# Optimization experiments

Measured on AMD Instinct MI355X. Metric: run time of the kernel, lower is better.

## Reference

```python
import jax, jax.numpy as jnp
import numpy as np

TEMPERATURE = 0.1
SIGMA = 1.0
NUM_CLASSES = 4
INF = 1e8
EPS = 1e-12


def _l2_normalize(x):
    n = jnp.sqrt(jnp.sum(x * x, axis=-1, keepdims=True))
    return x / jnp.maximum(n, EPS)


def _rbf_kernel(y, gamma):
    # y: [M, P] -> [M, M] exp(-gamma * ||yi - yj||^2)
    sq = jnp.sum(y * y, axis=-1)
    d2 = sq[:, None] + sq[None, :] - 2.0 * (y @ y.T)
    d2 = jnp.maximum(d2, 0.0)
    return jnp.exp(-gamma * d2)


def setup_inputs() -> dict:
    key = jax.random.key(0)
    k1, k2, k3, k4 = jax.random.split(key, 4)
    N, D = 2048, 512
    return {
        "z_i": jax.random.normal(k1, (N, D), dtype=jnp.float32),
        "z_j": jax.random.normal(k2, (N, D), dtype=jnp.float32),
        "labels": jax.random.randint(k3, (N,), 0, NUM_CLASSES, dtype=jnp.int64),
        "z_pos": jax.random.uniform(k4, (N, 1), dtype=jnp.float32),
    }


def reference(z_i, z_j, labels, z_pos):
    N = z_i.shape[0]
    zi = _l2_normalize(z_i)
    zj = _l2_normalize(z_j)

    eye_n = jnp.eye(N, dtype=zi.dtype)
    sim_zii = (zi @ zi.T) / TEMPERATURE - INF * eye_n
    sim_zjj = (zj @ zj.T) / TEMPERATURE - INF * eye_n
    sim_zij = (zi @ zj.T) / TEMPERATURE

    # label agreement mask over the 2N x 2N augmented batch
    labs = jax.nn.one_hot(labels, NUM_CLASSES, dtype=jnp.float32)
    L = jnp.concatenate([labs, labs], axis=0)          # [2N, C]
    eye_2n = jnp.eye(2 * N, dtype=jnp.float32)
    mask = (L @ L.T) * (1.0 - eye_2n)

    # RBF kernel weights over positional labels (detached in original)
    all_pos = jnp.tile(z_pos.reshape(N, -1), (2, 1))   # [2N, P]
    gamma = 1.0 / (2.0 * SIGMA ** 2)
    weights = _rbf_kernel(all_pos, gamma) * (1.0 - eye_2n)

    final_weights = weights * mask
    # NB: torch broadcasting divides column j by rowsum[j]; matrix is symmetric
    final_weights = final_weights / final_weights.sum(axis=1)

    top = jnp.concatenate([sim_zii, sim_zij], axis=1)
    bot = jnp.concatenate([sim_zij.T, sim_zjj], axis=1)
    sim_Z = jnp.concatenate([top, bot], axis=0)        # [2N, 2N]

    log_sim_Z = jax.nn.log_softmax(sim_Z, axis=1)
    loss = (-1.0 / N) * jnp.sum(log_sim_Z * final_weights)
    return loss
```

## Files before the change

### kernel.cpp

```cpp
#include <hip/hip_runtime.h>
#include <hip/hip_bf16.h>

#define D 512
#define INV_T 10.0f
#define INF_VAL 1e8f

#define BM 128
#define BN 128
#define BK 64
#define KSTEPS (D / BK)
#define NTB 32
#define NBLK (NTB * (NTB + 1) / 2)
#define NCHUNK 64

typedef short bf16x8 __attribute__((ext_vector_type(8)));
typedef float f32x4 __attribute__((ext_vector_type(4)));

typedef __attribute__((address_space(3))) unsigned int lds_uint;
typedef __attribute__((address_space(1))) unsigned int gbl_uint;

__device__ __forceinline__ void async_copy16(const ushort* gsrc, ushort* ldst) {
  __builtin_amdgcn_global_load_lds((const gbl_uint*)gsrc, (lds_uint*)ldst, 16, 0, 0);
}

__device__ inline float wave_reduce_sum(float v) {
#pragma unroll
  for (int off = 32; off > 0; off >>= 1) v += __shfl_xor(v, off);
  return v;
}

__device__ __forceinline__ ushort f2bf(float x) {
  __hip_bfloat16 h = __float2bfloat16(x);
  return *reinterpret_cast<ushort*>(&h);
}

__global__ __launch_bounds__(256) void k_prep(const float* __restrict__ zi,
                                              const float* __restrict__ zj,
                                              ushort* __restrict__ zb,
                                              const int* __restrict__ labels,
                                              const float* __restrict__ zpos,
                                              float* __restrict__ sinv, int N) {
  int b = blockIdx.x;
  if (b < 1024) {
    int wv = threadIdx.x >> 6, lane = threadIdx.x & 63;
    int row = b * 4 + wv;
    const float* src = (row < N) ? (zi + (size_t)row * D) : (zj + (size_t)(row - N) * D);
    const float4* s4 = reinterpret_cast<const float4*>(src);
    float4 v0 = s4[lane];
    float4 v1 = s4[lane + 64];
    float ss = 0.f;
    ss = fmaf(v0.x, v0.x, ss); ss = fmaf(v0.y, v0.y, ss);
    ss = fmaf(v0.z, v0.z, ss); ss = fmaf(v0.w, v0.w, ss);
    ss = fmaf(v1.x, v1.x, ss); ss = fmaf(v1.y, v1.y, ss);
    ss = fmaf(v1.z, v1.z, ss); ss = fmaf(v1.w, v1.w, ss);
    ss = wave_reduce_sum(ss);
    float sc = 1.0f / fmaxf(sqrtf(ss), 1e-12f);
    ushort4 o0 = {f2bf(v0.x * sc), f2bf(v0.y * sc), f2bf(v0.z * sc), f2bf(v0.w * sc)};
    ushort4 o1 = {f2bf(v1.x * sc), f2bf(v1.y * sc), f2bf(v1.z * sc), f2bf(v1.w * sc)};
    ushort4* dst = reinterpret_cast<ushort4*>(zb + (size_t)row * D);
    dst[lane] = o0;
    dst[lane + 64] = o1;
  } else {
    __shared__ float scratch[4];
    int j = b - 1024;
    int lj = labels[j];
    float pj = zpos[j];
    float s = 0.f;
    for (int i = threadIdx.x; i < N; i += 256) {
      if (labels[i] == lj) {
        float d = zpos[i] - pj;
        s += __expf(-0.5f * d * d);
      }
    }
    s = wave_reduce_sum(s);
    int lane = threadIdx.x & 63, wv = threadIdx.x >> 6;
    if (lane == 0) scratch[wv] = s;
    __syncthreads();
    if (threadIdx.x == 0) {
      float t = scratch[0] + scratch[1] + scratch[2] + scratch[3];
      sinv[j] = 1.0f / (2.0f * t - 1.0f);
    }
  }
}

__global__ __launch_bounds__(256) void k_tt(const int* __restrict__ labels,
                                            const float* __restrict__ zpos,
                                            const float* __restrict__ sinv,
                                            float* __restrict__ tt, int N) {
  __shared__ float scratch[4];
  int i = blockIdx.x;
  int li = labels[i];
  float pi = zpos[i];
  float s = 0.f;
  for (int j = threadIdx.x; j < N; j += 256) {
    if (labels[j] == li) {
      float d = zpos[j] - pi;
      s += __expf(-0.5f * d * d) * sinv[j];
    }
  }
  s = wave_reduce_sum(s);
  int lane = threadIdx.x & 63, wv = threadIdx.x >> 6;
  if (lane == 0) scratch[wv] = s;
  __syncthreads();
  if (threadIdx.x == 0) {
    tt[i] = scratch[0] + scratch[1] + scratch[2] + scratch[3];
  }
}

__global__ __launch_bounds__(256, 2) void k_gemm(
    const ushort* __restrict__ zb, const int* __restrict__ labels,
    const float* __restrict__ zpos, const float* __restrict__ sinv,
    float* __restrict__ s_ws, float* __restrict__ c_ws, int N) {
  __shared__ __align__(16) ushort sT[2][2][BM * BK];

  const int tid = threadIdx.x;
  const int lane = tid & 63;
  const int wv = tid >> 6;
  const int wr = wv >> 1;
  const int wc = wv & 1;
  const int colq = lane & 15;
  const int laneg = lane >> 4;
  const int twoN = 2 * N;

  const int bid = blockIdx.x;
  int L = (bid & 7) * (NBLK / 8) + (bid >> 3);
  int u = L, rt = 0;
  while (u >= NTB - rt) { u -= NTB - rt; ++rt; }
  const int ct = rt + u;
  const bool diag = (rt == ct);
  const int rowBase = rt * BM;
  const int colBase = ct * BN;

  const int srow = lane >> 3;
  const int sslot = (lane & 7) ^ srow;

  f32x4 acc[4][4] = {};

  {
#pragma unroll
    for (int q = 0; q < 4; ++q) {
      int rloc = wv * 32 + q * 8;
      async_copy16(zb + (size_t)(rowBase + rloc + srow) * D + 0 * BK + sslot * 8,
                   (ushort*)sT[0][0] + rloc * BK);
      if (!diag)
        async_copy16(zb + (size_t)(colBase + rloc + srow) * D + 0 * BK + sslot * 8,
                     (ushort*)sT[0][1] + rloc * BK);
    }
  }
  __syncthreads();

  int cur = 0;
#pragma unroll
  for (int kt = 0; kt < KSTEPS; ++kt) {
    if (kt + 1 < KSTEPS) {
#pragma unroll
      for (int q = 0; q < 4; ++q) {
        int rloc = wv * 32 + q * 8;
        async_copy16(zb + (size_t)(rowBase + rloc + srow) * D + (kt + 1) * BK + sslot * 8,
                     (ushort*)sT[cur ^ 1][0] + rloc * BK);
        if (!diag)
          async_copy16(zb + (size_t)(colBase + rloc + srow) * D + (kt + 1) * BK + sslot * 8,
                       (ushort*)sT[cur ^ 1][1] + rloc * BK);
      }
    }

    const char* Ab = reinterpret_cast<const char*>(sT[cur][0]);
    const char* Bb = diag ? Ab : reinterpret_cast<const char*>(sT[cur][1]);
#pragma unroll
    for (int kk = 0; kk < 2; ++kk) {
      bf16x8 a[4], b[4];
      const int slot = kk * 4 + laneg;
#pragma unroll
      for (int rf = 0; rf < 4; ++rf) {
        int r = wr * 64 + rf * 16 + colq;
        a[rf] = *reinterpret_cast<const bf16x8*>(Ab + r * 128 + (slot ^ (r & 7)) * 16);
      }
#pragma unroll
      for (int cf = 0; cf < 4; ++cf) {
        int c = wc * 64 + cf * 16 + colq;
        b[cf] = *reinterpret_cast<const bf16x8*>(Bb + c * 128 + (slot ^ (c & 7)) * 16);
      }
#pragma unroll
      for (int rf = 0; rf < 4; ++rf)
#pragma unroll
        for (int cf = 0; cf < 4; ++cf)
          acc[rf][cf] = __builtin_amdgcn_mfma_f32_16x16x32_bf16(a[rf], b[cf], acc[rf][cf], 0, 0, 0);
    }

    if (kt + 1 < KSTEPS) {
      __syncthreads();
      cur ^= 1;
    }
  }

  const int wRowBase = rowBase + wr * 64;
  const int wColBase = colBase + wc * 64;
  const int rmodBase = (wRowBase >= N) ? wRowBase - N : wRowBase;
  const int cmodBase = (wColBase >= N) ? wColBase - N : wColBase;

  float rpos[16], rsinv[16];
  unsigned rlab = 0;
#pragma unroll
  for (int rf = 0; rf < 4; ++rf)
#pragma unroll
    for (int rg = 0; rg < 4; ++rg) {
      int idx = rf * 4 + rg;
      int r = rmodBase + rf * 16 + laneg * 4 + rg;
      rpos[idx] = zpos[r];
      rsinv[idx] = sinv[r];
      rlab |= ((unsigned)labels[r] & 3u) << (idx * 2);
    }

  float s_p[16], c_p[16], sc_p[4], cc_p[4];
#pragma unroll
  for (int i = 0; i < 16; ++i) { s_p[i] = 0.f; c_p[i] = 0.f; }

#pragma unroll
  for (int cf = 0; cf < 4; ++cf) {
    int jc = cmodBase + cf * 16 + colq;
    int lc = labels[jc];
    float pc = zpos[jc];
    float si = sinv[jc];
    int col = wColBase + cf * 16 + colq;
    float scf = 0.f, ccf = 0.f;
#pragma unroll
    for (int rf = 0; rf < 4; ++rf)
#pragma unroll
      for (int rg = 0; rg < 4; ++rg) {
        int idx = rf * 4 + rg;
        int row = wRowBase + rf * 16 + laneg * 4 + rg;
        float sim = acc[rf][cf][rg] * INV_T;
        bool dg = (row == col);
        if (dg) sim = -INF_VAL;
        float e = __expf(sim - 10.f);
        s_p[idx] += e;
        scf += e;
        int lr = (int)((rlab >> (idx * 2)) & 3u);
        if (lr == lc && !dg) {
          float d = rpos[idx] - pc;
          float w = __expf(-0.5f * d * d);
          c_p[idx] = fmaf(w * si, sim, c_p[idx]);
          ccf = fmaf(w * rsinv[idx], sim, ccf);
        }
      }
    sc_p[cf] = scf;
    cc_p[cf] = ccf;
  }

#pragma unroll
  for (int idx = 0; idx < 16; ++idx) {
#pragma unroll
    for (int off = 1; off < 16; off <<= 1) {
      s_p[idx] += __shfl_xor(s_p[idx], off);
      c_p[idx] += __shfl_xor(c_p[idx], off);
    }
  }
  if (colq == 0) {
    int cc = ct * 2 + wc;
#pragma unroll
    for (int rf = 0; rf < 4; ++rf)
#pragma unroll
      for (int rg = 0; rg < 4; ++rg) {
        int idx = rf * 4 + rg;
        int row = wRowBase + rf * 16 + laneg * 4 + rg;
        s_ws[(size_t)cc * twoN + row] = s_p[idx];
        c_ws[(size_t)cc * twoN + row] = c_p[idx];
      }
  }

  if (!diag) {
#pragma unroll
    for (int cf = 0; cf < 4; ++cf) {
      sc_p[cf] += __shfl_xor(sc_p[cf], 16);
      sc_p[cf] += __shfl_xor(sc_p[cf], 32);
      cc_p[cf] += __shfl_xor(cc_p[cf], 16);
      cc_p[cf] += __shfl_xor(cc_p[cf], 32);
    }
    if (laneg == 0) {
      int cct = rt * 2 + wr;
#pragma unroll
      for (int cf = 0; cf < 4; ++cf) {
        int rowt = wColBase + cf * 16 + colq;
        s_ws[(size_t)cct * twoN + rowt] = sc_p[cf];
        c_ws[(size_t)cct * twoN + rowt] = cc_p[cf];
      }
    }
  }
}

__global__ __launch_bounds__(256) void k_combine(const float* __restrict__ s_ws,
                                                 const float* __restrict__ c_ws,
                                                 const float* __restrict__ sinv,
                                                 const float* __restrict__ tt,
                                                 float* __restrict__ partial, int N) {
  int a = blockIdx.x * 256 + threadIdx.x;
  int twoN = 2 * N;
  if (a >= twoN) return;
  float s = 0.f, c = 0.f;
  for (int cc = 0; cc < NCHUNK; ++cc) {
    s += s_ws[(size_t)cc * twoN + a];
    c += c_ws[(size_t)cc * twoN + a];
  }
  int ir = (a >= N) ? a - N : a;
  float lse = 10.f + logf(s);
  float wsum = 2.f * tt[ir] - sinv[ir];
  partial[a] = c - wsum * lse;
}

__global__ __launch_bounds__(256) void k_final(const float* __restrict__ partial,
                                               float* __restrict__ out, int N) {
  __shared__ float scratch[4];
  float s = 0.f;
  for (int a = threadIdx.x; a < 2 * N; a += 256) s += partial[a];
  s = wave_reduce_sum(s);
  int lane = threadIdx.x & 63, wv = threadIdx.x >> 6;
  if (lane == 0) scratch[wv] = s;
  __syncthreads();
  if (threadIdx.x == 0) {
    float t = scratch[0] + scratch[1] + scratch[2] + scratch[3];
    out[0] = (-1.0f / (float)N) * t;
  }
}

extern "C" void kernel_launch(void* const* d_in, const int* in_sizes, int n_in,
                              void* d_out, int out_size, void* d_ws, size_t ws_size,
                              hipStream_t stream) {
  (void)n_in; (void)out_size; (void)ws_size;
  const float* zi = (const float*)d_in[0];
  const float* zj = (const float*)d_in[1];
  const int* labels = (const int*)d_in[2];
  const float* zpos = (const float*)d_in[3];
  float* out = (float*)d_out;

  const int N = in_sizes[2];
  const int twoN = 2 * N;

  char* wsb = (char*)d_ws;
  ushort* zb = (ushort*)wsb;
  float* sinv = (float*)(wsb + (size_t)twoN * D * 2);
  float* tt = sinv + N;
  float* s_ws = tt + N;
  float* c_ws = s_ws + (size_t)NCHUNK * twoN;
  float* partial = c_ws + (size_t)NCHUNK * twoN;

  k_prep<<<1024 + 2048, 256, 0, stream>>>(zi, zj, zb, labels, zpos, sinv, N);
  k_tt<<<N, 256, 0, stream>>>(labels, zpos, sinv, tt, N);
  k_gemm<<<NBLK, 256, 0, stream>>>(zb, labels, zpos, sinv, s_ws, c_ws, N);
  k_combine<<<(twoN + 255) / 256, 256, 0, stream>>>(s_ws, c_ws, sinv, tt, partial, N);
  k_final<<<1, 256, 0, stream>>>(partial, out, N);
}
```

Baseline: 56.72 us.

## Fold tt into GEMM launch, use 512-thread blocks, and reduce in combine

The tt computation moves into extra blocks of the GEMM launch, which removes one kernel launch. The GEMM now runs 512-thread blocks in which each wave holds a 32x64 output subtile, and it uses explicit vmcnt waits and raw barriers for the double buffer. Diagonal tiles now load both operands. The partial-sum workspace grows to 192 slots, which prep zero-fills. The combine kernel does the per-block reduction itself, so the final kernel only sums 64 values. This trades more workspace traffic, plus a zero-fill pass, for fewer launches and higher occupancy.

```diff
diff --git a/kernel.cpp b/kernel.cpp
--- a/kernel.cpp
+++ b/kernel.cpp
@@ -6,12 +6,12 @@
 #define INF_VAL 1e8f
 
 #define BM 128
-#define BN 128
 #define BK 64
 #define KSTEPS (D / BK)
 #define NTB 32
 #define NBLK (NTB * (NTB + 1) / 2)
-#define NCHUNK 64
+#define TTBLK 64
+#define NSLOT 192
 
 typedef short bf16x8 __attribute__((ext_vector_type(8)));
 typedef float f32x4 __attribute__((ext_vector_type(4)));
@@ -39,7 +39,8 @@
                                               ushort* __restrict__ zb,
                                               const int* __restrict__ labels,
                                               const float* __restrict__ zpos,
-                                              float* __restrict__ sinv, int N) {
+                                              float* __restrict__ sinv,
+                                              float* __restrict__ zfill, int N) {
   int b = blockIdx.x;
   if (b < 1024) {
     int wv = threadIdx.x >> 6, lane = threadIdx.x & 63;
@@ -60,7 +61,7 @@
     ushort4* dst = reinterpret_cast<ushort4*>(zb + (size_t)row * D);
     dst[lane] = o0;
     dst[lane + 64] = o1;
-  } else {
+  } else if (b < 3072) {
     __shared__ float scratch[4];
     int j = b - 1024;
     int lj = labels[j];
@@ -80,99 +81,100 @@
       float t = scratch[0] + scratch[1] + scratch[2] + scratch[3];
       sinv[j] = 1.0f / (2.0f * t - 1.0f);
     }
-  }
-}
-
-__global__ __launch_bounds__(256) void k_tt(const int* __restrict__ labels,
-                                            const float* __restrict__ zpos,
-                                            const float* __restrict__ sinv,
-                                            float* __restrict__ tt, int N) {
-  __shared__ float scratch[4];
-  int i = blockIdx.x;
-  int li = labels[i];
-  float pi = zpos[i];
-  float s = 0.f;
-  for (int j = threadIdx.x; j < N; j += 256) {
-    if (labels[j] == li) {
-      float d = zpos[j] - pi;
-      s += __expf(-0.5f * d * d) * sinv[j];
-    }
-  }
-  s = wave_reduce_sum(s);
-  int lane = threadIdx.x & 63, wv = threadIdx.x >> 6;
-  if (lane == 0) scratch[wv] = s;
-  __syncthreads();
-  if (threadIdx.x == 0) {
-    tt[i] = scratch[0] + scratch[1] + scratch[2] + scratch[3];
-  }
-}
-
-__global__ __launch_bounds__(256, 2) void k_gemm(
+  } else {
+    size_t idx = (size_t)(b - 3072) * 256 + threadIdx.x;
+    float4 z = {0.f, 0.f, 0.f, 0.f};
+    reinterpret_cast<float4*>(zfill)[idx] = z;
+  }
+}
+
+__global__ __launch_bounds__(512, 4) void k_gemm(
     const ushort* __restrict__ zb, const int* __restrict__ labels,
     const float* __restrict__ zpos, const float* __restrict__ sinv,
+    float* __restrict__ tt,
     float* __restrict__ s_ws, float* __restrict__ c_ws, int N) {
+  const int tid = threadIdx.x;
+  const int bid = blockIdx.x;
+  const int twoN = 2 * N;
+
+  if (bid >= NBLK) {
+    int base = (bid - NBLK) * 32;
+    int i = base + (tid >> 4);
+    int part = tid & 15;
+    int li = labels[i];
+    float pi = zpos[i];
+    int seg = N >> 4;
+    float s = 0.f;
+    for (int j = part * seg; j < (part + 1) * seg; ++j) {
+      if (labels[j] == li) {
+        float d = zpos[j] - pi;
+        s += __expf(-0.5f * d * d) * sinv[j];
+      }
+    }
+    s += __shfl_xor(s, 1); s += __shfl_xor(s, 2);
+    s += __shfl_xor(s, 4); s += __shfl_xor(s, 8);
+    if (part == 0) tt[i] = s;
+    return;
+  }
+
   __shared__ __align__(16) ushort sT[2][2][BM * BK];
 
-  const int tid = threadIdx.x;
   const int lane = tid & 63;
   const int wv = tid >> 6;
   const int wr = wv >> 1;
   const int wc = wv & 1;
   const int colq = lane & 15;
   const int laneg = lane >> 4;
-  const int twoN = 2 * N;
-
-  const int bid = blockIdx.x;
+
   int L = (bid & 7) * (NBLK / 8) + (bid >> 3);
   int u = L, rt = 0;
   while (u >= NTB - rt) { u -= NTB - rt; ++rt; }
   const int ct = rt + u;
   const bool diag = (rt == ct);
   const int rowBase = rt * BM;
-  const int colBase = ct * BN;
+  const int colBase = ct * BM;
 
   const int srow = lane >> 3;
   const int sslot = (lane & 7) ^ srow;
 
-  f32x4 acc[4][4] = {};
-
-  {
-#pragma unroll
-    for (int q = 0; q < 4; ++q) {
-      int rloc = wv * 32 + q * 8;
-      async_copy16(zb + (size_t)(rowBase + rloc + srow) * D + 0 * BK + sslot * 8,
-                   (ushort*)sT[0][0] + rloc * BK);
-      if (!diag)
-        async_copy16(zb + (size_t)(colBase + rloc + srow) * D + 0 * BK + sslot * 8,
-                     (ushort*)sT[0][1] + rloc * BK);
-    }
-  }
-  __syncthreads();
-
+  f32x4 acc[2][4] = {};
+
+#define STAGE(buf, kt)                                                        \
+  {                                                                           \
+    _Pragma("unroll")                                                         \
+    for (int q = 0; q < 2; ++q) {                                             \
+      int rloc = wv * 16 + q * 8;                                             \
+      async_copy16(zb + (size_t)(rowBase + rloc + srow) * D + (kt) * BK +     \
+                       sslot * 8,                                             \
+                   (ushort*)sT[buf][0] + rloc * BK);                          \
+      async_copy16(zb + (size_t)(colBase + rloc + srow) * D + (kt) * BK +     \
+                       sslot * 8,                                             \
+                   (ushort*)sT[buf][1] + rloc * BK);                          \
+    }                                                                         \
+  }
+
+  STAGE(0, 0);
   int cur = 0;
 #pragma unroll
   for (int kt = 0; kt < KSTEPS; ++kt) {
     if (kt + 1 < KSTEPS) {
-#pragma unroll
-      for (int q = 0; q < 4; ++q) {
-        int rloc = wv * 32 + q * 8;
-        async_copy16(zb + (size_t)(rowBase + rloc + srow) * D + (kt + 1) * BK + sslot * 8,
-                     (ushort*)sT[cur ^ 1][0] + rloc * BK);
-        if (!diag)
-          async_copy16(zb + (size_t)(colBase + rloc + srow) * D + (kt + 1) * BK + sslot * 8,
-                       (ushort*)sT[cur ^ 1][1] + rloc * BK);
-      }
-    }
+      STAGE(cur ^ 1, kt + 1);
+      asm volatile("s_waitcnt vmcnt(4)" ::: "memory");
+    } else {
+      asm volatile("s_waitcnt vmcnt(0)" ::: "memory");
+    }
+    __builtin_amdgcn_s_barrier();
+    __builtin_amdgcn_sched_barrier(0);
 
     const char* Ab = reinterpret_cast<const char*>(sT[cur][0]);
-    const char* Bb = diag ? Ab : reinterpret_cast<const char*>(sT[cur][1]);
+    const char* Bb = reinterpret_cast<const char*>(sT[cur][1]);
 #pragma unroll
     for (int kk = 0; kk < 2; ++kk) {
-      bf16x8 a[4], b[4];
+      bf16x8 a[2], b[4];
       const int slot = kk * 4 + laneg;
 #pragma unroll
-      for (int rf = 0; rf < 4; ++rf) {
-        int r = wr * 64 + rf * 16 + colq;
+      for (int rf = 0; rf < 2; ++rf) {
+        int r = wr * 32 + rf * 16 + colq;
         a[rf] = *reinterpret_cast<const bf16x8*>(Ab + r * 128 + (slot ^ (r & 7)) * 16);
       }
 #pragma unroll
@@ -181,27 +183,26 @@
         b[cf] = *reinterpret_cast<const bf16x8*>(Bb + c * 128 + (slot ^ (c & 7)) * 16);
       }
 #pragma unroll
-      for (int rf = 0; rf < 4; ++rf)
+      for (int rf = 0; rf < 2; ++rf)
 #pragma unroll
         for (int cf = 0; cf < 4; ++cf)
           acc[rf][cf] = __builtin_amdgcn_mfma_f32_16x16x32_bf16(a[rf], b[cf], acc[rf][cf], 0, 0, 0);
     }
-
-    if (kt + 1 < KSTEPS) {
-      __syncthreads();
-      cur ^= 1;
-    }
-  }
-
-  const int wRowBase = rowBase + wr * 64;
+    __builtin_amdgcn_sched_barrier(0);
+    __builtin_amdgcn_s_barrier();
+    cur ^= 1;
+  }
+#undef STAGE
+
+  const int wRowBase = rowBase + wr * 32;
   const int wColBase = colBase + wc * 64;
   const int rmodBase = (wRowBase >= N) ? wRowBase - N : wRowBase;
   const int cmodBase = (wColBase >= N) ? wColBase - N : wColBase;
 
-  float rpos[16], rsinv[16];
+  float rpos[8], rsinv[8];
   unsigned rlab = 0;
 #pragma unroll
-  for (int rf = 0; rf < 4; ++rf)
+  for (int rf = 0; rf < 2; ++rf)
 #pragma unroll
     for (int rg = 0; rg < 4; ++rg) {
       int idx = rf * 4 + rg;
@@ -211,9 +212,9 @@
       rlab |= ((unsigned)labels[r] & 3u) << (idx * 2);
     }
 
-  float s_p[16], c_p[16], sc_p[4], cc_p[4];
-#pragma unroll
-  for (int i = 0; i < 16; ++i) { s_p[i] = 0.f; c_p[i] = 0.f; }
+  float s_p[8], c_p[8], sc_p[4], cc_p[4];
+#pragma unroll
+  for (int i = 0; i < 8; ++i) { s_p[i] = 0.f; c_p[i] = 0.f; }
 
 #pragma unroll
   for (int cf = 0; cf < 4; ++cf) {
@@ -224,7 +225,7 @@
     int col = wColBase + cf * 16 + colq;
     float scf = 0.f, ccf = 0.f;
 #pragma unroll
-    for (int rf = 0; rf < 4; ++rf)
+    for (int rf = 0; rf < 2; ++rf)
 #pragma unroll
       for (int rg = 0; rg < 4; ++rg) {
         int idx = rf * 4 + rg;
@@ -248,7 +249,7 @@
   }
 
 #pragma unroll
-  for (int idx = 0; idx < 16; ++idx) {
+  for (int idx = 0; idx < 8; ++idx) {
 #pragma unroll
     for (int off = 1; off < 16; off <<= 1) {
       s_p[idx] += __shfl_xor(s_p[idx], off);
@@ -256,15 +257,15 @@
     }
   }
   if (colq == 0) {
-    int cc = ct * 2 + wc;
-#pragma unroll
-    for (int rf = 0; rf < 4; ++rf)
+    int slot = ct * 2 + wc;
+#pragma unroll
+    for (int rf = 0; rf < 2; ++rf)
 #pragma unroll
       for (int rg = 0; rg < 4; ++rg) {
         int idx = rf * 4 + rg;
         int row = wRowBase + rf * 16 + laneg * 4 + rg;
-        s_ws[(size_t)cc * twoN + row] = s_p[idx];
-        c_ws[(size_t)cc * twoN + row] = c_p[idx];
+        s_ws[(size_t)slot * twoN + row] = s_p[idx];
+        c_ws[(size_t)slot * twoN + row] = c_p[idx];
       }
   }
 
@@ -277,12 +278,12 @@
       cc_p[cf] += __shfl_xor(cc_p[cf], 32);
     }
     if (laneg == 0) {
-      int cct = rt * 2 + wr;
+      int slot = 64 + rt * 4 + wr;
 #pragma unroll
       for (int cf = 0; cf < 4; ++cf) {
         int rowt = wColBase + cf * 16 + colq;
-        s_ws[(size_t)cct * twoN + rowt] = sc_p[cf];
-        c_ws[(size_t)cct * twoN + rowt] = cc_p[cf];
+        s_ws[(size_t)slot * twoN + rowt] = sc_p[cf];
+        c_ws[(size_t)slot * twoN + rowt] = cc_p[cf];
       }
     }
   }
@@ -292,34 +293,39 @@
                                                  const float* __restrict__ c_ws,
                                                  const float* __restrict__ sinv,
                                                  const float* __restrict__ tt,
-                                                 float* __restrict__ partial, int N) {
-  int a = blockIdx.x * 256 + threadIdx.x;
+                                                 float* __restrict__ bsum, int N) {
+  __shared__ float sS[4][64], sC[4][64];
+  int b = blockIdx.x, t = threadIdx.x;
+  int r = t & 63, g = t >> 6;
   int twoN = 2 * N;
-  if (a >= twoN) return;
+  int a = b * 64 + r;
   float s = 0.f, c = 0.f;
-  for (int cc = 0; cc < NCHUNK; ++cc) {
-    s += s_ws[(size_t)cc * twoN + a];
-    c += c_ws[(size_t)cc * twoN + a];
-  }
-  int ir = (a >= N) ? a - N : a;
-  float lse = 10.f + logf(s);
-  float wsum = 2.f * tt[ir] - sinv[ir];
-  partial[a] = c - wsum * lse;
-}
-
-__global__ __launch_bounds__(256) void k_final(const float* __restrict__ partial,
-                                               float* __restrict__ out, int N) {
-  __shared__ float scratch[4];
-  float s = 0.f;
-  for (int a = threadIdx.x; a < 2 * N; a += 256) s += partial[a];
+  for (int k = 0; k < NSLOT / 4; ++k) {
+    int sl = g * (NSLOT / 4) + k;
+    s += s_ws[(size_t)sl * twoN + a];
+    c += c_ws[(size_t)sl * twoN + a];
+  }
+  sS[g][r] = s;
+  sC[g][r] = c;
+  __syncthreads();
+  if (t < 64) {
+    float st = sS[0][t] + sS[1][t] + sS[2][t] + sS[3][t];
+    float ct = sC[0][t] + sC[1][t] + sC[2][t] + sC[3][t];
+    int aa = b * 64 + t;
+    int ir = (aa >= N) ? aa - N : aa;
+    float lse = 10.f + logf(st);
+    float wsum = 2.f * tt[ir] - sinv[ir];
+    float p = ct - wsum * lse;
+    p = wave_reduce_sum(p);
+    if (t == 0) bsum[b] = p;
+  }
+}
+
+__global__ __launch_bounds__(64) void k_final(const float* __restrict__ bsum,
+                                              float* __restrict__ out, int N) {
+  float s = bsum[threadIdx.x];
   s = wave_reduce_sum(s);
-  int lane = threadIdx.x & 63, wv = threadIdx.x >> 6;
-  if (lane == 0) scratch[wv] = s;
-  __syncthreads();
-  if (threadIdx.x == 0) {
-    float t = scratch[0] + scratch[1] + scratch[2] + scratch[3];
-    out[0] = (-1.0f / (float)N) * t;
-  }
+  if (threadIdx.x == 0) out[0] = (-1.0f / (float)N) * s;
 }
 
 extern "C" void kernel_launch(void* const* d_in, const int* in_sizes, int n_in,
@@ -340,12 +346,11 @@
   float* sinv = (float*)(wsb + (size_t)twoN * D * 2);
   float* tt = sinv + N;
   float* s_ws = tt + N;
-  float* c_ws = s_ws + (size_t)NCHUNK * twoN;
-  float* partial = c_ws + (size_t)NCHUNK * twoN;
-
-  k_prep<<<1024 + 2048, 256, 0, stream>>>(zi, zj, zb, labels, zpos, sinv, N);
-  k_tt<<<N, 256, 0, stream>>>(labels, zpos, sinv, tt, N);
-  k_gemm<<<NBLK, 256, 0, stream>>>(zb, labels, zpos, sinv, s_ws, c_ws, N);
-  k_combine<<<(twoN + 255) / 256, 256, 0, stream>>>(s_ws, c_ws, sinv, tt, partial, N);
-  k_final<<<1, 256, 0, stream>>>(partial, out, N);
-}
+  float* c_ws = s_ws + (size_t)NSLOT * twoN;
+  float* bsum = c_ws + (size_t)NSLOT * twoN;
+
+  k_prep<<<1024 + 2048 + 1536, 256, 0, stream>>>(zi, zj, zb, labels, zpos, sinv, s_ws, N);
+  k_gemm<<<NBLK + TTBLK, 512, 0, stream>>>(zb, labels, zpos, sinv, tt, s_ws, c_ws, N);
+  k_combine<<<twoN / 64, 256, 0, stream>>>(s_ws, c_ws, sinv, tt, bsum, N);
+  k_final<<<1, 64, 0, stream>>>(bsum, out, N);
+}
```

Measured after the change: 78.92 us. 1.39x slower.
